# Kernel optimization log

Hardware: AMD Instinct MI355X
Metric: run time of the kernel (lower is better)

## Reference

```python
import jax, jax.numpy as jnp
import numpy as np

BETA = 1.0
NUM_CLASSES = 64  # upper bound on region ids per image (mask.max()+1 in original)


def setup_inputs() -> dict:
    key = jax.random.key(0)
    k1, k2, k3 = jax.random.split(key, 3)
    B, C, H, W = 16, 3, 512, 512
    inp = jax.random.normal(k1, (B, C, H, W), dtype=jnp.float32)
    tgt = jax.random.normal(k2, (B, C, H, W), dtype=jnp.float32)
    mask = jax.random.randint(k3, (B, H, W), 0, NUM_CLASSES, dtype=jnp.int32)
    return {"input": inp, "target": tgt, "mask": mask}


def reference(input, target, mask):
    B, C, H, W = input.shape
    # per-element L1 (reduce=False)
    loss = jnp.abs(input - target)                      # [B,C,H,W]
    w = jax.lax.stop_gradient(loss)                     # detached copy
    # segmented mean over (channels x region pixels) per (batch, class)
    seg = (jnp.arange(B, dtype=mask.dtype)[:, None, None] * NUM_CLASSES + mask).reshape(-1)  # [B*H*W]
    w_csum = w.sum(axis=1).reshape(-1)                  # sum over channels per pixel, [B*H*W]
    sums = jax.ops.segment_sum(w_csum, seg, num_segments=B * NUM_CLASSES)
    cnts = jax.ops.segment_sum(jnp.ones_like(w_csum), seg, num_segments=B * NUM_CLASSES)
    avg = sums / jnp.maximum(cnts * C, 1.0)             # mean over C*area elements; safe for empty regions
    # broadcast region averages back (same value across channels)
    weight = avg[seg].reshape(B, 1, H, W)               # [B,1,H,W]
    weight = weight / jnp.max(weight)
    weight = jnp.clip(weight, 0.0, 1.0)
    return jnp.mean(loss * (weight * BETA + 1.0))
```

## Files before the change

### kernel.cpp

```cpp
#include <hip/hip_runtime.h>
#include <hip/hip_bf16.h>

#define NUM_CLASSES 64
#define BATCH 16
#define CHAN 3
#define HW (512 * 512)
#define BPB 128
#define THREADS 256
#define NREP 4
#define CPAD 8

__global__ __launch_bounds__(THREADS) void frl_accum(
    const float4* __restrict__ inp,
    const float4* __restrict__ tgt,
    const int4* __restrict__ mask,
    float* __restrict__ g_sum,
    unsigned int* __restrict__ g_cnt)
{
    __shared__ float s_sum[NREP][NUM_CLASSES + CPAD];
    __shared__ unsigned int s_cnt[NREP][NUM_CLASSES + CPAD];
    const int t = threadIdx.x;
    for (int i = t; i < NREP * (NUM_CLASSES + CPAD); i += THREADS) {
        ((float*)s_sum)[i] = 0.0f;
        ((unsigned int*)s_cnt)[i] = 0u;
    }
    __syncthreads();

    const int b   = blockIdx.x / BPB;
    const int blk = blockIdx.x % BPB;
    const int GPB = HW / 4 / BPB;
    const int rep = t & (NREP - 1);

    const int g0    = blk * GPB;
    const int cbase = b * (CHAN * HW / 4);
    const int mbase = b * (HW / 4);
    const int CS    = HW / 4;

    const int ga = g0 + t;
    const int gb = g0 + t + THREADS;

    const int4 ma = mask[mbase + ga];
    const int4 mb = mask[mbase + gb];
    const float4 ia0 = inp[cbase + 0 * CS + ga];
    const float4 ta0 = tgt[cbase + 0 * CS + ga];
    const float4 ia1 = inp[cbase + 1 * CS + ga];
    const float4 ta1 = tgt[cbase + 1 * CS + ga];
    const float4 ia2 = inp[cbase + 2 * CS + ga];
    const float4 ta2 = tgt[cbase + 2 * CS + ga];
    const float4 ib0 = inp[cbase + 0 * CS + gb];
    const float4 tb0 = tgt[cbase + 0 * CS + gb];
    const float4 ib1 = inp[cbase + 1 * CS + gb];
    const float4 tb1 = tgt[cbase + 1 * CS + gb];
    const float4 ib2 = inp[cbase + 2 * CS + gb];
    const float4 tb2 = tgt[cbase + 2 * CS + gb];

    const float la0 = fabsf(ia0.x - ta0.x) + fabsf(ia1.x - ta1.x) + fabsf(ia2.x - ta2.x);
    const float la1 = fabsf(ia0.y - ta0.y) + fabsf(ia1.y - ta1.y) + fabsf(ia2.y - ta2.y);
    const float la2 = fabsf(ia0.z - ta0.z) + fabsf(ia1.z - ta1.z) + fabsf(ia2.z - ta2.z);
    const float la3 = fabsf(ia0.w - ta0.w) + fabsf(ia1.w - ta1.w) + fabsf(ia2.w - ta2.w);
    const float lb0 = fabsf(ib0.x - tb0.x) + fabsf(ib1.x - tb1.x) + fabsf(ib2.x - tb2.x);
    const float lb1 = fabsf(ib0.y - tb0.y) + fabsf(ib1.y - tb1.y) + fabsf(ib2.y - tb2.y);
    const float lb2 = fabsf(ib0.z - tb0.z) + fabsf(ib1.z - tb1.z) + fabsf(ib2.z - tb2.z);
    const float lb3 = fabsf(ib0.w - tb0.w) + fabsf(ib1.w - tb1.w) + fabsf(ib2.w - tb2.w);

    atomicAdd(&s_sum[rep][ma.x], la0);
    atomicAdd(&s_sum[rep][ma.y], la1);
    atomicAdd(&s_sum[rep][ma.z], la2);
    atomicAdd(&s_sum[rep][ma.w], la3);
    atomicAdd(&s_sum[rep][mb.x], lb0);
    atomicAdd(&s_sum[rep][mb.y], lb1);
    atomicAdd(&s_sum[rep][mb.z], lb2);
    atomicAdd(&s_sum[rep][mb.w], lb3);
    atomicAdd(&s_cnt[rep][ma.x], 1u);
    atomicAdd(&s_cnt[rep][ma.y], 1u);
    atomicAdd(&s_cnt[rep][ma.z], 1u);
    atomicAdd(&s_cnt[rep][ma.w], 1u);
    atomicAdd(&s_cnt[rep][mb.x], 1u);
    atomicAdd(&s_cnt[rep][mb.y], 1u);
    atomicAdd(&s_cnt[rep][mb.z], 1u);
    atomicAdd(&s_cnt[rep][mb.w], 1u);

    __syncthreads();
    if (t < NUM_CLASSES) {
        float fs = 0.0f;
        unsigned int cs = 0u;
        #pragma unroll
        for (int r = 0; r < NREP; ++r) { fs += s_sum[r][t]; cs += s_cnt[r][t]; }
        atomicAdd(&g_sum[b * NUM_CLASSES + t], fs);
        atomicAdd(&g_cnt[b * NUM_CLASSES + t], cs);
    }
}

__global__ __launch_bounds__(256) void frl_finalize(
    const float* __restrict__ g_sum,
    const unsigned int* __restrict__ g_cnt,
    float* __restrict__ out)
{
    const int NSEG = BATCH * NUM_CLASSES;
    __shared__ float s_avg[BATCH * NUM_CLASSES];
    __shared__ float red[256];
    const int t = threadIdx.x;

    float lmax = 0.0f;
    for (int s = t; s < NSEG; s += 256) {
        const float sum = g_sum[s];
        const float cnt = (float)g_cnt[s];
        const float avg = sum / fmaxf(cnt * (float)CHAN, 1.0f);
        s_avg[s] = avg;
        lmax = fmaxf(lmax, avg);
    }
    red[t] = lmax;
    __syncthreads();
    for (int off = 128; off > 0; off >>= 1) {
        if (t < off) red[t] = fmaxf(red[t], red[t + off]);
        __syncthreads();
    }
    const float maxavg = fmaxf(red[0], 1e-30f);
    __syncthreads();

    float part = 0.0f;
    for (int s = t; s < NSEG; s += 256) {
        const float w = fminf(fmaxf(s_avg[s] / maxavg, 0.0f), 1.0f);
        part += g_sum[s] * (1.0f + w);
    }
    red[t] = part;
    __syncthreads();
    for (int off = 128; off > 0; off >>= 1) {
        if (t < off) red[t] += red[t + off];
        __syncthreads();
    }
    if (t == 0) {
        out[0] = red[0] / (float)((size_t)BATCH * CHAN * HW);
    }
}

extern "C" void kernel_launch(void* const* d_in, const int* in_sizes, int n_in,
                              void* d_out, int out_size, void* d_ws, size_t ws_size,
                              hipStream_t stream) {
    const float4* inp = (const float4*)d_in[0];
    const float4* tgt = (const float4*)d_in[1];
    const int4* mask  = (const int4*)d_in[2];

    float* g_sum        = (float*)d_ws;
    unsigned int* g_cnt = (unsigned int*)((char*)d_ws + BATCH * NUM_CLASSES * sizeof(float));

    hipMemsetAsync(d_ws, 0, 2 * BATCH * NUM_CLASSES * sizeof(float), stream);
    frl_accum<<<BATCH * BPB, THREADS, 0, stream>>>(inp, tgt, mask, g_sum, g_cnt);
    frl_finalize<<<1, 256, 0, stream>>>(g_sum, g_cnt, (float*)d_out);
}
```

Measured before the change: 142.6 us.

## Halve accum blocks and loop over four chunks with register prefetch

```diff
diff --git a/kernel.cpp b/kernel.cpp
--- a/kernel.cpp
+++ b/kernel.cpp
@@ -5,12 +5,13 @@
 #define BATCH 16
 #define CHAN 3
 #define HW (512 * 512)
-#define BPB 128
+#define BPB 64
 #define THREADS 256
+#define NITER 4
 #define NREP 4
 #define CPAD 8
 
-__global__ __launch_bounds__(THREADS) void frl_accum(
+__global__ __launch_bounds__(THREADS, 4) void frl_accum(
     const float4* __restrict__ inp,
     const float4* __restrict__ tgt,
     const int4* __restrict__ mask,
@@ -31,54 +32,60 @@
     const int GPB = HW / 4 / BPB;
     const int rep = t & (NREP - 1);
 
-    const int g0    = blk * GPB;
+    const int g0    = blk * GPB + t;
     const int cbase = b * (CHAN * HW / 4);
     const int mbase = b * (HW / 4);
     const int CS    = HW / 4;
 
-    const int ga = g0 + t;
-    const int gb = g0 + t + THREADS;
+    int4   m_c;
+    float4 i0_c, t0_c, i1_c, t1_c, i2_c, t2_c;
+    {
+        const int g = g0;
+        m_c  = mask[mbase + g];
+        i0_c = inp[cbase + 0 * CS + g];
+        t0_c = tgt[cbase + 0 * CS + g];
+        i1_c = inp[cbase + 1 * CS + g];
+        t1_c = tgt[cbase + 1 * CS + g];
+        i2_c = inp[cbase + 2 * CS + g];
+        t2_c = tgt[cbase + 2 * CS + g];
+    }
 
-    const int4 ma = mask[mbase + ga];
-    const int4 mb = mask[mbase + gb];
-    const float4 ia0 = inp[cbase + 0 * CS + ga];
-    const float4 ta0 = tgt[cbase + 0 * CS + ga];
-    const float4 ia1 = inp[cbase + 1 * CS + ga];
-    const float4 ta1 = tgt[cbase + 1 * CS + ga];
-    const float4 ia2 = inp[cbase + 2 * CS + ga];
-    const float4 ta2 = tgt[cbase + 2 * CS + ga];
-    const float4 ib0 = inp[cbase + 0 * CS + gb];
-    const float4 tb0 = tgt[cbase + 0 * CS + gb];
-    const float4 ib1 = inp[cbase + 1 * CS + gb];
-    const float4 tb1 = tgt[cbase + 1 * CS + gb];
-    const float4 ib2 = inp[cbase + 2 * CS + gb];
-    const float4 tb2 = tgt[cbase + 2 * CS + gb];
+    #pragma unroll
+    for (int it = 0; it < NITER; ++it) {
+        int4   m_n;
+        float4 i0_n, t0_n, i1_n, t1_n, i2_n, t2_n;
+        if (it + 1 < NITER) {
+            const int g = g0 + (it + 1) * THREADS;
+            m_n  = mask[mbase + g];
+            i0_n = inp[cbase + 0 * CS + g];
+            t0_n = tgt[cbase + 0 * CS + g];
+            i1_n = inp[cbase + 1 * CS + g];
+            t1_n = tgt[cbase + 1 * CS + g];
+            i2_n = inp[cbase + 2 * CS + g];
+            t2_n = tgt[cbase + 2 * CS + g];
+        }
 
-    const float la0 = fabsf(ia0.x - ta0.x) + fabsf(ia1.x - ta1.x) + fabsf(ia2.x - ta2.x);
-    const float la1 = fabsf(ia0.y - ta0.y) + fabsf(ia1.y - ta1.y) + fabsf(ia2.y - ta2.y);
-    const float la2 = fabsf(ia0.z - ta0.z) + fabsf(ia1.z - ta1.z) + fabsf(ia2.z - ta2.z);
-    const float la3 = fabsf(ia0.w - ta0.w) + fabsf(ia1.w - ta1.w) + fabsf(ia2.w - ta2.w);
-    const float lb0 = fabsf(ib0.x - tb0.x) + fabsf(ib1.x - tb1.x) + fabsf(ib2.x - tb2.x);
-    const float lb1 = fabsf(ib0.y - tb0.y) + fabsf(ib1.y - tb1.y) + fabsf(ib2.y - tb2.y);
-    const float lb2 = fabsf(ib0.z - tb0.z) + fabsf(ib1.z - tb1.z) + fabsf(ib2.z - tb2.z);
-    const float lb3 = fabsf(ib0.w - tb0.w) + fabsf(ib1.w - tb1.w) + fabsf(ib2.w - tb2.w);
+        const float l0 = fabsf(i0_c.x - t0_c.x) + fabsf(i1_c.x - t1_c.x) + fabsf(i2_c.x - t2_c.x);
+        const float l1 = fabsf(i0_c.y - t0_c.y) + fabsf(i1_c.y - t1_c.y) + fabsf(i2_c.y - t2_c.y);
+        const float l2 = fabsf(i0_c.z - t0_c.z) + fabsf(i1_c.z - t1_c.z) + fabsf(i2_c.z - t2_c.z);
+        const float l3 = fabsf(i0_c.w - t0_c.w) + fabsf(i1_c.w - t1_c.w) + fabsf(i2_c.w - t2_c.w);
 
-    atomicAdd(&s_sum[rep][ma.x], la0);
-    atomicAdd(&s_sum[rep][ma.y], la1);
-    atomicAdd(&s_sum[rep][ma.z], la2);
-    atomicAdd(&s_sum[rep][ma.w], la3);
-    atomicAdd(&s_sum[rep][mb.x], lb0);
-    atomicAdd(&s_sum[rep][mb.y], lb1);
-    atomicAdd(&s_sum[rep][mb.z], lb2);
-    atomicAdd(&s_sum[rep][mb.w], lb3);
-    atomicAdd(&s_cnt[rep][ma.x], 1u);
-    atomicAdd(&s_cnt[rep][ma.y], 1u);
-    atomicAdd(&s_cnt[rep][ma.z], 1u);
-    atomicAdd(&s_cnt[rep][ma.w], 1u);
-    atomicAdd(&s_cnt[rep][mb.x], 1u);
-    atomicAdd(&s_cnt[rep][mb.y], 1u);
-    atomicAdd(&s_cnt[rep][mb.z], 1u);
-    atomicAdd(&s_cnt[rep][mb.w], 1u);
+        atomicAdd(&s_sum[rep][m_c.x], l0);
+        atomicAdd(&s_sum[rep][m_c.y], l1);
+        atomicAdd(&s_sum[rep][m_c.z], l2);
+        atomicAdd(&s_sum[rep][m_c.w], l3);
+        atomicAdd(&s_cnt[rep][m_c.x], 1u);
+        atomicAdd(&s_cnt[rep][m_c.y], 1u);
+        atomicAdd(&s_cnt[rep][m_c.z], 1u);
+        atomicAdd(&s_cnt[rep][m_c.w], 1u);
+
+        if (it + 1 < NITER) {
+            m_c  = m_n;
+            i0_c = i0_n; t0_c = t0_n;
+            i1_c = i1_n; t1_c = t1_n;
+            i2_c = i2_n; t2_c = t2_n;
+        }
+    }
 
     __syncthreads();
     if (t < NUM_CLASSES) {
```

New measurement: 145.0 us. No clear change (+1.7%).
